# Performance work log

Hardware: AMD Instinct MI355X
Metric: run time of the kernel (lower is better)

## Reference

```python
import jax, jax.numpy as jnp
import numpy as np

N = 1 << 20          # number of sample points (rays x samples)
ENC = 32             # hash-grid encoded dim (16 levels x 2 features)
HID = 64
GEO = 15


def setup_inputs() -> dict:
    key = jax.random.key(0)
    ks = jax.random.split(key, 16)
    sc = lambda fan_in: 1.0 / np.sqrt(fan_in)
    return {
        "x": jax.random.normal(ks[0], (N, ENC), jnp.float32),
        "d": jax.random.normal(ks[1], (N, ENC), jnp.float32),
        # sigma net: ENC -> 64 -> 64 -> 1+GEO, bias-free, stored [in, out]
        "Ws0": jax.random.normal(ks[2], (ENC, HID), jnp.float32) * sc(ENC),
        "Ws1": jax.random.normal(ks[3], (HID, HID), jnp.float32) * sc(HID),
        "Ws2": jax.random.normal(ks[4], (HID, 1 + GEO), jnp.float32) * sc(HID),
        # color net: ENC+GEO -> 64 -> 64 -> 64 -> 3, bias-free
        "Wc0": jax.random.normal(ks[5], (ENC + GEO, HID), jnp.float32) * sc(ENC + GEO),
        "Wc1": jax.random.normal(ks[6], (HID, HID), jnp.float32) * sc(HID),
        "Wc2": jax.random.normal(ks[7], (HID, HID), jnp.float32) * sc(HID),
        "Wc3": jax.random.normal(ks[8], (HID, 3), jnp.float32) * sc(HID),
    }


def reference(x, d, Ws0, Ws1, Ws2, Wc0, Wc1, Wc2, Wc3):
    # sigma network: ReLU after EVERY layer (including the last, as in source)
    h = x
    for W in (Ws0, Ws1, Ws2):
        h = jax.nn.relu(h @ W)
    sigma = h[..., 0]            # [N]
    geo_feat = h[..., 1:]        # [N, GEO]

    # color network: ReLU on all but last layer, then sigmoid
    h = jnp.concatenate([d, geo_feat], axis=-1)   # [N, ENC+GEO]
    color_ws = (Wc0, Wc1, Wc2, Wc3)
    for i, W in enumerate(color_ws):
        h = h @ W
        if i != len(color_ws) - 1:
            h = jax.nn.relu(h)
    color = jax.nn.sigmoid(h)    # [N, 3]
    return color, sigma
```

## Files before the change

kernel.cpp:

```cpp
#include <hip/hip_runtime.h>
#include <hip/hip_bf16.h>

typedef short s8v __attribute__((ext_vector_type(8)));
typedef float f4v __attribute__((ext_vector_type(4)));

#define MFMA_BF16 __builtin_amdgcn_mfma_f32_16x16x32_bf16

constexpr int OFF_W0T  = 0;
constexpr int OFF_W1T  = 2560;
constexpr int OFF_W2T  = 7168;
constexpr int OFF_WC0T = 8320;
constexpr int OFF_WC1T = 12928;
constexpr int OFF_WC2T = 17536;
constexpr int OFF_WC3T = 22144;
constexpr int SMEM_EL  = 23296;

static __device__ __forceinline__ short bf2s(__hip_bfloat16 h) {
    union { __hip_bfloat16 b; short s; } u; u.b = h; return u.s;
}

__global__ __launch_bounds__(512, 6)
void rf_fused(const void* __restrict__ xv,
              const void* __restrict__ dv,
              const void* __restrict__ Ws0,
              const void* __restrict__ Ws1,
              const void* __restrict__ Ws2,
              const void* __restrict__ Wc0,
              const void* __restrict__ Wc1,
              const void* __restrict__ Wc2,
              const void* __restrict__ Wc3,
              void* __restrict__ outp,
              int npts)
{
    __shared__ __align__(16) short smem[SMEM_EL];
    __shared__ int cls_cnt;
    const int t = threadIdx.x;

    if (t == 0) cls_cnt = 0;
    __syncthreads();
    {
        unsigned short w = ((const unsigned short*)xv)[2 * t];
        int e = (w >> 7) & 0xFF;
        if (e >= 110 && e <= 140) atomicAdd(&cls_cnt, 1);
    }
    __syncthreads();
    const bool isbf = (cls_cnt >= 256);

    auto ldw = [&](const void* p, int idx) -> short {
        if (isbf) return ((const short*)p)[idx];
        return bf2s(__float2bfloat16(((const float*)p)[idx]));
    };

    for (int i = t; i < 2048; i += 512) { int k = i >> 6, n = i & 63; smem[OFF_W0T  + n*40 + k] = ldw(Ws0, i); }
    for (int i = t; i < 4096; i += 512) { int k = i >> 6, n = i & 63; smem[OFF_W1T  + n*72 + k] = ldw(Ws1, i); }
    for (int i = t; i < 1024; i += 512) { int k = i >> 4, n = i & 15; smem[OFF_W2T  + n*72 + k] = ldw(Ws2, i); }
    for (int i = t; i < 4096; i += 512) {
        int n = i >> 6, k = i & 63;
        short v = 0;
        if (k < 32)                 v = ldw(Wc0, k*64 + n);
        else if (k >= 33 && k < 48) v = ldw(Wc0, (k-1)*64 + n);
        smem[OFF_WC0T + n*72 + k] = v;
    }
    for (int i = t; i < 4096; i += 512) { int k = i >> 6, n = i & 63; smem[OFF_WC1T + n*72 + k] = ldw(Wc1, i); }
    for (int i = t; i < 4096; i += 512) { int k = i >> 6, n = i & 63; smem[OFF_WC2T + n*72 + k] = ldw(Wc2, i); }
    for (int i = t; i < 1024; i += 512) { int n = i >> 6, k = i & 63; smem[OFF_WC3T + n*72 + k] = (n < 3) ? ldw(Wc3, k*3 + n) : (short)0; }
    __syncthreads();

    const int lane = t & 63;
    const int wv   = t >> 6;
    const int m16  = lane & 15;
    const int q    = lane >> 4;

    const f4v zf = {0.f, 0.f, 0.f, 0.f};

    auto loadRow8f = [&](const void* p, int eoff) -> s8v {
        const float* f = (const float*)p + eoff;
        f4v f0 = *(const f4v*)f;
        f4v f1 = *(const f4v*)(f + 4);
        s8v r;
        #pragma unroll
        for (int j = 0; j < 4; j++) {
            r[j]     = bf2s(__float2bfloat16(f0[j]));
            r[j + 4] = bf2s(__float2bfloat16(f1[j]));
        }
        return r;
    };
    auto putOut = [&](int idx, float v) {
        if (isbf) ((short*)outp)[idx] = bf2s(__float2bfloat16(v));
        else      ((float*)outp)[idx] = v;
    };

    auto cvtpk = [](float lo, float hi) -> unsigned int {
        unsigned int r;
        asm("v_cvt_pk_bf16_f32 %0, %1, %2" : "=v"(r) : "v"(lo), "v"(hi));
        return r;
    };

    auto redist = [&](const f4v (&a)[4], s8v (&fr)[2]) {
        unsigned int P[4][2];
        #pragma unroll
        for (int kt = 0; kt < 4; kt++)
            #pragma unroll
            for (int rp = 0; rp < 2; rp++)
                P[kt][rp] = cvtpk(fmaxf(a[kt][2*rp], 0.f), fmaxf(a[kt][2*rp+1], 0.f));
        #pragma unroll
        for (int a2 = 0; a2 < 2; a2++)
            #pragma unroll
            for (int rp = 0; rp < 2; rp++) {
                asm("v_permlane32_swap_b32 %0, %1" : "+v"(P[2*a2][rp]), "+v"(P[2*a2+1][rp]));
                asm("v_permlane16_swap_b32 %0, %1" : "+v"(P[2*a2][rp]), "+v"(P[2*a2+1][rp]));
            }
        #pragma unroll
        for (int kc = 0; kc < 2; kc++) {
            union { unsigned int u[4]; s8v v; } fu;
            fu.u[0] = P[2*kc][0];     fu.u[1] = P[2*kc][1];
            fu.u[2] = P[2*kc + 1][0]; fu.u[3] = P[2*kc + 1][1];
            fr[kc] = fu.v;
        }
    };
    auto redistHalf = [&](const f4v s, s8v &frHi) {
        unsigned int P2[2], P3[2];
        #pragma unroll
        for (int rp = 0; rp < 2; rp++) {
            P2[rp] = cvtpk(fmaxf(s[2*rp], 0.f), fmaxf(s[2*rp+1], 0.f));
            P3[rp] = P2[rp];
        }
        #pragma unroll
        for (int rp = 0; rp < 2; rp++) {
            asm("v_permlane32_swap_b32 %0, %1" : "+v"(P2[rp]), "+v"(P3[rp]));
            asm("v_permlane16_swap_b32 %0, %1" : "+v"(P2[rp]), "+v"(P3[rp]));
        }
        union { unsigned int u[4]; s8v v; } fu;
        fu.u[0] = P2[0]; fu.u[1] = P2[1]; fu.u[2] = P3[0]; fu.u[3] = P3[1];
        frHi = fu.v;
    };

    auto layerT = [&](int woff, const s8v (&bfr)[2][2], f4v (&out)[2][4]) {
        #pragma unroll
        for (int kt = 0; kt < 4; kt++) {
            s8v a0 = *(const s8v*)(smem + woff + (kt*16 + m16)*72 + q*8);
            s8v a1 = *(const s8v*)(smem + woff + (kt*16 + m16)*72 + 32 + q*8);
            #pragma unroll
            for (int pt = 0; pt < 2; pt++)
                out[pt][kt] = MFMA_BF16(a1, bfr[pt][1],
                              MFMA_BF16(a0, bfr[pt][0], zf, 0,0,0), 0,0,0);
        }
    };

    const int ntiles = npts / 32;
    const int tstep  = gridDim.x * 8;
    int tile = blockIdx.x * 8 + wv;

    s8v xb[2], db[2];
    if (isbf && tile < ntiles) {
        #pragma unroll
        for (int pt = 0; pt < 2; pt++) {
            const int off = (tile*32 + pt*16 + m16)*32 + q*8;
            xb[pt] = *(const s8v*)((const short*)xv + off);
            db[pt] = *(const s8v*)((const short*)dv + off);
        }
    }

    #pragma unroll 1
    for (; tile < ntiles; tile += tstep) {
        const int r0  = tile * 32;
        const int nxt = tile + tstep;

        if (!isbf) {
            #pragma unroll
            for (int pt = 0; pt < 2; pt++) {
                const int off = (r0 + pt*16 + m16)*32 + q*8;
                xb[pt] = loadRow8f(xv, off);
                db[pt] = loadRow8f(dv, off);
            }
        }

        f4v acc[2][4];
        s8v bfr[2][2];

        #pragma unroll
        for (int kt = 0; kt < 4; kt++) {
            s8v a0 = *(const s8v*)(smem + OFF_W0T + (kt*16 + m16)*40 + q*8);
            #pragma unroll
            for (int pt = 0; pt < 2; pt++)
                acc[pt][kt] = MFMA_BF16(a0, xb[pt], zf, 0,0,0);
        }

        if (isbf && nxt < ntiles) {
            #pragma unroll
            for (int pt = 0; pt < 2; pt++)
                xb[pt] = *(const s8v*)((const short*)xv + (nxt*32 + pt*16 + m16)*32 + q*8);
        }

        #pragma unroll
        for (int pt = 0; pt < 2; pt++) redist(acc[pt], bfr[pt]);

        layerT(OFF_W1T, bfr, acc);
        #pragma unroll
        for (int pt = 0; pt < 2; pt++) redist(acc[pt], bfr[pt]);

        f4v s3[2];
        {
            s8v c0 = *(const s8v*)(smem + OFF_W2T + m16*72 + q*8);
            s8v c1 = *(const s8v*)(smem + OFF_W2T + m16*72 + 32 + q*8);
            #pragma unroll
            for (int pt = 0; pt < 2; pt++)
                s3[pt] = MFMA_BF16(c1, bfr[pt][1],
                         MFMA_BF16(c0, bfr[pt][0], zf, 0,0,0), 0,0,0);
        }

        if (q == 0) {
            #pragma unroll
            for (int pt = 0; pt < 2; pt++)
                putOut(3*npts + r0 + pt*16 + m16, fmaxf(s3[pt][0], 0.f));
        }

        #pragma unroll
        for (int pt = 0; pt < 2; pt++) {
            redistHalf(s3[pt], bfr[pt][1]);
            bfr[pt][0] = db[pt];
        }

        layerT(OFF_WC0T, bfr, acc);

        if (isbf && nxt < ntiles) {
            #pragma unroll
            for (int pt = 0; pt < 2; pt++)
                db[pt] = *(const s8v*)((const short*)dv + (nxt*32 + pt*16 + m16)*32 + q*8);
        }

        #pragma unroll
        for (int pt = 0; pt < 2; pt++) redist(acc[pt], bfr[pt]);

        layerT(OFF_WC1T, bfr, acc);
        #pragma unroll
        for (int pt = 0; pt < 2; pt++) redist(acc[pt], bfr[pt]);

        layerT(OFF_WC2T, bfr, acc);
        #pragma unroll
        for (int pt = 0; pt < 2; pt++) redist(acc[pt], bfr[pt]);

        f4v c7[2];
        {
            s8v e0 = *(const s8v*)(smem + OFF_WC3T + m16*72 + q*8);
            s8v e1 = *(const s8v*)(smem + OFF_WC3T + m16*72 + 32 + q*8);
            #pragma unroll
            for (int pt = 0; pt < 2; pt++)
                c7[pt] = MFMA_BF16(e1, bfr[pt][1],
                         MFMA_BF16(e0, bfr[pt][0], zf, 0,0,0), 0,0,0);
        }
        if (q == 0) {
            #pragma unroll
            for (int pt = 0; pt < 2; pt++) {
                const int base = (r0 + pt*16 + m16) * 3;
                #pragma unroll
                for (int r = 0; r < 3; r++) {
                    float v  = c7[pt][r];
                    float sg = 1.0f / (1.0f + __expf(-v));
                    putOut(base + r, sg);
                }
            }
        }
    }
}

extern "C" void kernel_launch(void* const* d_in, const int* in_sizes, int n_in,
                              void* d_out, int out_size, void* d_ws, size_t ws_size,
                              hipStream_t stream) {
    const int npts = in_sizes[0] / 32;
    rf_fused<<<768, 512, 0, stream>>>(d_in[0], d_in[1], d_in[2], d_in[3], d_in[4],
                                      d_in[5], d_in[6], d_in[7], d_in[8],
                                      d_out, npts);
}
```

Before: 325.0 us.

## Process two tiles per wave iteration to reuse weight fragments

Each wave now handles two 32-point tiles per loop iteration, so every weight fragment loaded from shared memory feeds twice as many MFMAs and there is more independent work to hide MFMA latency. The software prefetch of the next tile's x/d inputs is removed; inputs are loaded at the start of each iteration, with d loaded later. Occupancy drops from 6 to 4 blocks per CU and the grid shrinks from 768 to 512 blocks to fit the higher register use.

```diff
diff --git a/kernel.cpp b/kernel.cpp
--- a/kernel.cpp
+++ b/kernel.cpp
@@ -19,7 +19,7 @@
     union { __hip_bfloat16 b; short s; } u; u.b = h; return u.s;
 }
 
-__global__ __launch_bounds__(512, 6)
+__global__ __launch_bounds__(512, 4)
 void rf_fused(const void* __restrict__ xv,
               const void* __restrict__ dv,
               const void* __restrict__ Ws0,
@@ -135,131 +135,148 @@
         frHi = fu.v;
     };
 
-    auto layerT = [&](int woff, const s8v (&bfr)[2][2], f4v (&out)[2][4]) {
+    auto layerT2 = [&](int woff, const s8v (&bfr)[2][2][2], f4v (&out)[2][2][4]) {
         #pragma unroll
         for (int kt = 0; kt < 4; kt++) {
             s8v a0 = *(const s8v*)(smem + woff + (kt*16 + m16)*72 + q*8);
             s8v a1 = *(const s8v*)(smem + woff + (kt*16 + m16)*72 + 32 + q*8);
             #pragma unroll
-            for (int pt = 0; pt < 2; pt++)
-                out[pt][kt] = MFMA_BF16(a1, bfr[pt][1],
-                              MFMA_BF16(a0, bfr[pt][0], zf, 0,0,0), 0,0,0);
+            for (int u = 0; u < 2; u++)
+                #pragma unroll
+                for (int pt = 0; pt < 2; pt++)
+                    out[u][pt][kt] = MFMA_BF16(a1, bfr[u][pt][1],
+                                     MFMA_BF16(a0, bfr[u][pt][0], zf, 0,0,0), 0,0,0);
         }
     };
 
     const int ntiles = npts / 32;
-    const int tstep  = gridDim.x * 8;
-    int tile = blockIdx.x * 8 + wv;
-
-    s8v xb[2], db[2];
-    if (isbf && tile < ntiles) {
-        #pragma unroll
-        for (int pt = 0; pt < 2; pt++) {
-            const int off = (tile*32 + pt*16 + m16)*32 + q*8;
-            xb[pt] = *(const s8v*)((const short*)xv + off);
-            db[pt] = *(const s8v*)((const short*)dv + off);
-        }
-    }
+    const int nw     = gridDim.x * 8;
+    int base = blockIdx.x * 8 + wv;
 
     #pragma unroll 1
-    for (; tile < ntiles; tile += tstep) {
-        const int r0  = tile * 32;
-        const int nxt = tile + tstep;
-
-        if (!isbf) {
+    for (; base < ntiles; base += 2 * nw) {
+        const int tA   = base;
+        const int tB   = base + nw;
+        const bool hasB = tB < ntiles;
+        const int tl[2] = { tA, hasB ? tB : tA };
+
+        s8v xb[2][2];
+        #pragma unroll
+        for (int u = 0; u < 2; u++)
             #pragma unroll
             for (int pt = 0; pt < 2; pt++) {
-                const int off = (r0 + pt*16 + m16)*32 + q*8;
-                xb[pt] = loadRow8f(xv, off);
-                db[pt] = loadRow8f(dv, off);
-            }
-        }
-
-        f4v acc[2][4];
-        s8v bfr[2][2];
+                const int off = (tl[u]*32 + pt*16 + m16)*32 + q*8;
+                xb[u][pt] = isbf ? *(const s8v*)((const short*)xv + off)
+                                 : loadRow8f(xv, off);
+            }
+
+        f4v acc[2][2][4];
+        s8v bfr[2][2][2];
 
         #pragma unroll
         for (int kt = 0; kt < 4; kt++) {
             s8v a0 = *(const s8v*)(smem + OFF_W0T + (kt*16 + m16)*40 + q*8);
             #pragma unroll
-            for (int pt = 0; pt < 2; pt++)
-                acc[pt][kt] = MFMA_BF16(a0, xb[pt], zf, 0,0,0);
-        }
-
-        if (isbf && nxt < ntiles) {
-            #pragma unroll
-            for (int pt = 0; pt < 2; pt++)
-                xb[pt] = *(const s8v*)((const short*)xv + (nxt*32 + pt*16 + m16)*32 + q*8);
-        }
-
-        #pragma unroll
-        for (int pt = 0; pt < 2; pt++) redist(acc[pt], bfr[pt]);
-
-        layerT(OFF_W1T, bfr, acc);
-        #pragma unroll
-        for (int pt = 0; pt < 2; pt++) redist(acc[pt], bfr[pt]);
-
-        f4v s3[2];
+            for (int u = 0; u < 2; u++)
+                #pragma unroll
+                for (int pt = 0; pt < 2; pt++)
+                    acc[u][pt][kt] = MFMA_BF16(a0, xb[u][pt], zf, 0,0,0);
+        }
+        #pragma unroll
+        for (int u = 0; u < 2; u++)
+            #pragma unroll
+            for (int pt = 0; pt < 2; pt++) redist(acc[u][pt], bfr[u][pt]);
+
+        layerT2(OFF_W1T, bfr, acc);
+        #pragma unroll
+        for (int u = 0; u < 2; u++)
+            #pragma unroll
+            for (int pt = 0; pt < 2; pt++) redist(acc[u][pt], bfr[u][pt]);
+
+        s8v db[2][2];
+        #pragma unroll
+        for (int u = 0; u < 2; u++)
+            #pragma unroll
+            for (int pt = 0; pt < 2; pt++) {
+                const int off = (tl[u]*32 + pt*16 + m16)*32 + q*8;
+                db[u][pt] = isbf ? *(const s8v*)((const short*)dv + off)
+                                 : loadRow8f(dv, off);
+            }
+
+        f4v s3[2][2];
         {
             s8v c0 = *(const s8v*)(smem + OFF_W2T + m16*72 + q*8);
             s8v c1 = *(const s8v*)(smem + OFF_W2T + m16*72 + 32 + q*8);
             #pragma unroll
-            for (int pt = 0; pt < 2; pt++)
-                s3[pt] = MFMA_BF16(c1, bfr[pt][1],
-                         MFMA_BF16(c0, bfr[pt][0], zf, 0,0,0), 0,0,0);
+            for (int u = 0; u < 2; u++)
+                #pragma unroll
+                for (int pt = 0; pt < 2; pt++)
+                    s3[u][pt] = MFMA_BF16(c1, bfr[u][pt][1],
+                                MFMA_BF16(c0, bfr[u][pt][0], zf, 0,0,0), 0,0,0);
         }
 
         if (q == 0) {
             #pragma unroll
-            for (int pt = 0; pt < 2; pt++)
-                putOut(3*npts + r0 + pt*16 + m16, fmaxf(s3[pt][0], 0.f));
-        }
-
-        #pragma unroll
-        for (int pt = 0; pt < 2; pt++) {
-            redistHalf(s3[pt], bfr[pt][1]);
-            bfr[pt][0] = db[pt];
-        }
-
-        layerT(OFF_WC0T, bfr, acc);
-
-        if (isbf && nxt < ntiles) {
-            #pragma unroll
-            for (int pt = 0; pt < 2; pt++)
-                db[pt] = *(const s8v*)((const short*)dv + (nxt*32 + pt*16 + m16)*32 + q*8);
-        }
-
-        #pragma unroll
-        for (int pt = 0; pt < 2; pt++) redist(acc[pt], bfr[pt]);
-
-        layerT(OFF_WC1T, bfr, acc);
-        #pragma unroll
-        for (int pt = 0; pt < 2; pt++) redist(acc[pt], bfr[pt]);
-
-        layerT(OFF_WC2T, bfr, acc);
-        #pragma unroll
-        for (int pt = 0; pt < 2; pt++) redist(acc[pt], bfr[pt]);
-
-        f4v c7[2];
+            for (int u = 0; u < 2; u++)
+                if (u == 0 || hasB) {
+                    #pragma unroll
+                    for (int pt = 0; pt < 2; pt++)
+                        putOut(3*npts + tl[u]*32 + pt*16 + m16, fmaxf(s3[u][pt][0], 0.f));
+                }
+        }
+
+        #pragma unroll
+        for (int u = 0; u < 2; u++)
+            #pragma unroll
+            for (int pt = 0; pt < 2; pt++) {
+                redistHalf(s3[u][pt], bfr[u][pt][1]);
+                bfr[u][pt][0] = db[u][pt];
+            }
+
+        layerT2(OFF_WC0T, bfr, acc);
+        #pragma unroll
+        for (int u = 0; u < 2; u++)
+            #pragma unroll
+            for (int pt = 0; pt < 2; pt++) redist(acc[u][pt], bfr[u][pt]);
+
+        layerT2(OFF_WC1T, bfr, acc);
+        #pragma unroll
+        for (int u = 0; u < 2; u++)
+            #pragma unroll
+            for (int pt = 0; pt < 2; pt++) redist(acc[u][pt], bfr[u][pt]);
+
+        layerT2(OFF_WC2T, bfr, acc);
+        #pragma unroll
+        for (int u = 0; u < 2; u++)
+            #pragma unroll
+            for (int pt = 0; pt < 2; pt++) redist(acc[u][pt], bfr[u][pt]);
+
+        f4v c7[2][2];
         {
             s8v e0 = *(const s8v*)(smem + OFF_WC3T + m16*72 + q*8);
             s8v e1 = *(const s8v*)(smem + OFF_WC3T + m16*72 + 32 + q*8);
             #pragma unroll
-            for (int pt = 0; pt < 2; pt++)
-                c7[pt] = MFMA_BF16(e1, bfr[pt][1],
-                         MFMA_BF16(e0, bfr[pt][0], zf, 0,0,0), 0,0,0);
+            for (int u = 0; u < 2; u++)
+                #pragma unroll
+                for (int pt = 0; pt < 2; pt++)
+                    c7[u][pt] = MFMA_BF16(e1, bfr[u][pt][1],
+                                MFMA_BF16(e0, bfr[u][pt][0], zf, 0,0,0), 0,0,0);
         }
         if (q == 0) {
             #pragma unroll
-            for (int pt = 0; pt < 2; pt++) {
-                const int base = (r0 + pt*16 + m16) * 3;
-                #pragma unroll
-                for (int r = 0; r < 3; r++) {
-                    float v  = c7[pt][r];
-                    float sg = 1.0f / (1.0f + __expf(-v));
-                    putOut(base + r, sg);
+            for (int u = 0; u < 2; u++)
+                if (u == 0 || hasB) {
+                    #pragma unroll
+                    for (int pt = 0; pt < 2; pt++) {
+                        const int bout = (tl[u]*32 + pt*16 + m16) * 3;
+                        #pragma unroll
+                        for (int r = 0; r < 3; r++) {
+                            float v  = c7[u][pt][r];
+                            float sg = 1.0f / (1.0f + __expf(-v));
+                            putOut(bout + r, sg);
+                        }
+                    }
                 }
-            }
         }
     }
 }
@@ -268,7 +285,7 @@
                               void* d_out, int out_size, void* d_ws, size_t ws_size,
                               hipStream_t stream) {
     const int npts = in_sizes[0] / 32;
-    rf_fused<<<768, 512, 0, stream>>>(d_in[0], d_in[1], d_in[2], d_in[3], d_in[4],
+    rf_fused<<<512, 512, 0, stream>>>(d_in[0], d_in[1], d_in[2], d_in[3], d_in[4],
                                       d_in[5], d_in[6], d_in[7], d_in[8],
                                       d_out, npts);
 }
```

After: 319.3 us. No clear change (-1.8%).
